# Optimization experiments

Measured on AMD Instinct MI355X. Metric: run time of the kernel, lower is better.

The kernel has to match this reference:

```python
import jax, jax.numpy as jnp
import numpy as np

B, S = 4096, 4096
NEG_INF = -1e30


def _conv1d_same(x, w, pad):
    # x: [B, S], w: [K] -> cross-correlation with zero padding, like torch F.conv1d
    out = jax.lax.conv_general_dilated(
        x[:, None, :], w[None, None, :], (1,), [(pad, pad)],
        dimension_numbers=("NCH", "OIH", "NCH"))
    return out[:, 0, :]


def setup_inputs() -> dict:
    key = jax.random.key(0)
    kx, kl, k1, k2, k3 = jax.random.split(key, 5)
    x = jax.random.normal(kx, (B, S), dtype=jnp.float32)
    length = jax.random.randint(kl, (B,), 1, S + 1, dtype=jnp.int32)
    w1 = 0.01 * jax.random.normal(k1, (3,), dtype=jnp.float32)
    w2 = 0.01 * jax.random.normal(k2, (5,), dtype=jnp.float32)
    w3 = 0.01 * jax.random.normal(k3, (7,), dtype=jnp.float32)
    return {"x": x, "length": length, "w1": w1, "w2": w2, "w3": w3}


def reference(x, length, w1, w2, w3):
    # mask out padding beyond each sample's length; zeroing x beyond length makes
    # the 'same'-padded conv identical to per-sample conv on the truncated sequence
    pos = jnp.arange(S)
    mask = pos[None, :] < length[:, None]          # [B, S]
    xm = jnp.where(mask, x, 0.0)

    def branch(w, pad):
        logits = _conv1d_same(xm, w, pad)          # [B, S]
        logits = jnp.where(mask, logits, NEG_INF)  # softmax only over valid positions
        qw = jax.nn.softmax(logits, axis=-1)
        return jnp.sum(qw * xm, axis=-1)           # [B]

    s1 = branch(w1, 1)
    s2 = branch(w2, 2)
    s3 = branch(w3, 3)
    fused = (s1 + s2 + s3) / 3.0
    return fused[:, None]                          # [B, 1]
```

## Files before the change

kernel.cpp:

```cpp
#include <hip/hip_runtime.h>

#define SEQ   4096
#define CHUNK 256
#define WPR   4

struct Ch { float4 vl, vm, vr; };

__global__ __launch_bounds__(256) void msr_kernel(
    const float* __restrict__ x, const int* __restrict__ length,
    const float* __restrict__ w1, const float* __restrict__ w2,
    const float* __restrict__ w3, float* __restrict__ out)
{
    __shared__ float red[WPR][8];

    const int row  = blockIdx.x;
    const int tid  = threadIdx.x;
    const int wave = tid >> 6;
    const int lane = tid & 63;
    const int L    = length[row];
    const int nch  = (L + CHUNK - 1) >> 8;

    const float a0=w1[0],a1=w1[1],a2=w1[2];
    const float b0=w2[0],b1=w2[1],b2=w2[2],b3=w2[3],b4=w2[4];
    const float c0=w3[0],c1=w3[1],c2=w3[2],c3=w3[3],c4=w3[4],c5=w3[5],c6=w3[6];

    const float* __restrict__ xr = x + (size_t)row * SEQ;

    float d1=0.f,n1=0.f,d2=0.f,n2=0.f,d3=0.f,n3=0.f;

    auto load = [&](int it) -> Ch {
        Ch c;
        c.vl = make_float4(0.f,0.f,0.f,0.f);
        c.vm = c.vl; c.vr = c.vl;
        const int e = (it << 8) + (lane << 2);
        if (e < L) {
            c.vm = *reinterpret_cast<const float4*>(xr + e);
            if (e >= 4)        c.vl = *reinterpret_cast<const float4*>(xr + e - 4);
            if (e + 4 < SEQ)   c.vr = *reinterpret_cast<const float4*>(xr + e + 4);
        }
        return c;
    };

    auto proc = [&](const Ch c, int it) {
        const int start = it << 8;
        const int e     = start + (lane << 2);
        float s[12] = {c.vl.x,c.vl.y,c.vl.z,c.vl.w,
                       c.vm.x,c.vm.y,c.vm.z,c.vm.w,
                       c.vr.x,c.vr.y,c.vr.z,c.vr.w};
        const bool safe = (start + CHUNK + 4) <= L;
        if (!safe) {
            #pragma unroll
            for (int k = 4; k < 12; ++k)
                if (e - 4 + k >= L) s[k] = 0.f;
        }
        #pragma unroll
        for (int j = 0; j < 4; ++j) {
            const float xm3=s[j+1], xm2=s[j+2], xm1=s[j+3], x0=s[j+4],
                        xp1=s[j+5], xp2=s[j+6], xp3=s[j+7];
            const float l1 = fmaf(a0,xm1, fmaf(a1,x0, a2*xp1));
            const float l2 = fmaf(b0,xm2, fmaf(b1,xm1, fmaf(b2,x0,
                             fmaf(b3,xp1, b4*xp2))));
            const float l3 = fmaf(c0,xm3, fmaf(c1,xm2, fmaf(c2,xm1, fmaf(c3,x0,
                             fmaf(c4,xp1, fmaf(c5,xp2, c6*xp3))))));
            float E1 = __expf(l1), E2 = __expf(l2), E3 = __expf(l3);
            if (!safe) {
                const float m = (e + j < L) ? 1.f : 0.f;
                E1 *= m; E2 *= m; E3 *= m;
            }
            d1 += E1; n1 = fmaf(E1, x0, n1);
            d2 += E2; n2 = fmaf(E2, x0, n2);
            d3 += E3; n3 = fmaf(E3, x0, n3);
        }
    };

    Ch A = load(wave);
    Ch B = load(wave + WPR);
    for (int it = wave; it < nch; it += WPR) {
        Ch C = load(it + 2 * WPR);
        proc(A, it);
        A = B; B = C;
    }

    #pragma unroll
    for (int off = 32; off > 0; off >>= 1) {
        d1 += __shfl_xor(d1, off); n1 += __shfl_xor(n1, off);
        d2 += __shfl_xor(d2, off); n2 += __shfl_xor(n2, off);
        d3 += __shfl_xor(d3, off); n3 += __shfl_xor(n3, off);
    }
    if (lane == 0) {
        red[wave][0]=d1; red[wave][1]=n1; red[wave][2]=d2;
        red[wave][3]=n2; red[wave][4]=d3; red[wave][5]=n3;
    }
    __syncthreads();
    if (tid == 0) {
        float D1=0.f,N1=0.f,D2=0.f,N2=0.f,D3=0.f,N3=0.f;
        #pragma unroll
        for (int w = 0; w < WPR; ++w) {
            D1+=red[w][0]; N1+=red[w][1]; D2+=red[w][2];
            N2+=red[w][3]; D3+=red[w][4]; N3+=red[w][5];
        }
        out[row] = (N1/D1 + N2/D2 + N3/D3) * (1.0f/3.0f);
    }
}

extern "C" void kernel_launch(void* const* d_in, const int* in_sizes, int n_in,
                              void* d_out, int out_size, void* d_ws, size_t ws_size,
                              hipStream_t stream) {
    const float* x      = (const float*)d_in[0];
    const int*   length = (const int*)d_in[1];
    const float* w1     = (const float*)d_in[2];
    const float* w2     = (const float*)d_in[3];
    const float* w3     = (const float*)d_in[4];
    float*       out    = (float*)d_out;
    const int    Bn     = in_sizes[1];
    msr_kernel<<<Bn, 256, 0, stream>>>(x, length, w1, w2, w3, out);
}
```

Measured before the change: 21.29 us.

## Map one wave per row instead of one block per row

Each 64-lane wave now processes an entire row, with four rows per block, replacing the previous scheme where four waves split a row and reduced through shared memory and __syncthreads. This drops the shared-memory reduction and block barrier, and lets waves finish independently, which helps with the varying row lengths. In exchange, each wave walks up to 16 chunks serially with a prefetch depth of two, and the grid size is hardcoded to 1024 blocks, so it assumes B=4096.

```diff
diff --git a/kernel.cpp b/kernel.cpp
--- a/kernel.cpp
+++ b/kernel.cpp
@@ -2,7 +2,7 @@
 
 #define SEQ   4096
 #define CHUNK 256
-#define WPR   4
+#define NBLK  1024
 
 struct Ch { float4 vl, vm, vr; };
 
@@ -11,14 +11,10 @@
     const float* __restrict__ w1, const float* __restrict__ w2,
     const float* __restrict__ w3, float* __restrict__ out)
 {
-    __shared__ float red[WPR][8];
-
-    const int row  = blockIdx.x;
-    const int tid  = threadIdx.x;
-    const int wave = tid >> 6;
-    const int lane = tid & 63;
+    const int wave = threadIdx.x >> 6;
+    const int lane = threadIdx.x & 63;
+    const int row  = (blockIdx.x << 2) + wave;
     const int L    = length[row];
-    const int nch  = (L + CHUNK - 1) >> 8;
 
     const float a0=w1[0],a1=w1[1],a2=w1[2];
     const float b0=w2[0],b1=w2[1],b2=w2[2],b3=w2[3],b4=w2[4];
@@ -73,10 +69,11 @@
         }
     };
 
-    Ch A = load(wave);
-    Ch B = load(wave + WPR);
-    for (int it = wave; it < nch; it += WPR) {
-        Ch C = load(it + 2 * WPR);
+    const int nch = (L + CHUNK - 1) >> 8;
+    Ch A = load(0);
+    Ch B = load(1);
+    for (int it = 0; it < nch; ++it) {
+        Ch C = load(it + 2);
         proc(A, it);
         A = B; B = C;
     }
@@ -88,18 +85,7 @@
         d3 += __shfl_xor(d3, off); n3 += __shfl_xor(n3, off);
     }
     if (lane == 0) {
-        red[wave][0]=d1; red[wave][1]=n1; red[wave][2]=d2;
-        red[wave][3]=n2; red[wave][4]=d3; red[wave][5]=n3;
-    }
-    __syncthreads();
-    if (tid == 0) {
-        float D1=0.f,N1=0.f,D2=0.f,N2=0.f,D3=0.f,N3=0.f;
-        #pragma unroll
-        for (int w = 0; w < WPR; ++w) {
-            D1+=red[w][0]; N1+=red[w][1]; D2+=red[w][2];
-            N2+=red[w][3]; D3+=red[w][4]; N3+=red[w][5];
-        }
-        out[row] = (N1/D1 + N2/D2 + N3/D3) * (1.0f/3.0f);
+        out[row] = (n1/d1 + n2/d2 + n3/d3) * (1.0f/3.0f);
     }
 }
 
@@ -112,6 +98,5 @@
     const float* w2     = (const float*)d_in[3];
     const float* w3     = (const float*)d_in[4];
     float*       out    = (float*)d_out;
-    const int    Bn     = in_sizes[1];
-    msr_kernel<<<Bn, 256, 0, stream>>>(x, length, w1, w2, w3, out);
+    msr_kernel<<<NBLK, 256, 0, stream>>>(x, length, w1, w2, w3, out);
 }
```

New measurement: 27.14 us. +27.5%, slower.
